# Kernel tuning notes

Measured on AMD Instinct MI355X. Metric: run time of the kernel, lower is better.

The kernel has to match this reference:

```python
import jax, jax.numpy as jnp
import numpy as np

N, C, HEADS, NL = 2048, 64, 4, 4
DH = C // HEADS
EPS = 1e-8

def _pdist(pos):
    d2 = jnp.sum((pos[:, None, :] - pos[None, :, :]) ** 2, -1)
    return jnp.sqrt(d2 + 1e-12)

def _edge_weights(pos, adj):
    d = _pdist(pos)
    sigma = jnp.maximum((adj * d).sum() / jnp.maximum(adj.sum(), 1.0), 1e-6)
    return adj * jnp.exp(-(d * d) / (2.0 * sigma * sigma))

def _curvatures(pos, adj):
    deg = jnp.maximum(adj.sum(1), 1.0)
    delta = (adj @ pos) / deg[:, None] - pos          # umbrella Laplacian of coordinates
    H = 0.5 * jnp.linalg.norm(delta, axis=1)          # mean curvature proxy
    d = _pdist(pos)
    r = (adj * d).sum(1) / deg
    var = (adj * (d - r[:, None]) ** 2).sum(1) / deg
    s = jnp.sqrt(var + 1e-12)
    k1, k2 = H + s, H - s
    return dict(mean=H, gaussian=k1 * k2, principal_1=k1, principal_2=k2,
                shape_index=(2.0 / jnp.pi) * jnp.arctan((k1 + k2) / (k1 - k2 + 1e-6)),
                curvedness=jnp.sqrt(0.5 * (k1 ** 2 + k2 ** 2)))

def _ln(x, g, b):
    mu = x.mean(-1, keepdims=True)
    v = ((x - mu) ** 2).mean(-1, keepdims=True)
    return (x - mu) * jax.lax.rsqrt(v + 1e-5) * g + b

def _forward(positions, adj, Wc1, bc1, Wc2, bc2, Win, b_in,
             conv_Wself, conv_bself, conv_Wneigh, conv_bneigh, conv_res,
             diff_W, diff_b, rd_W1, rd_b1, rd_W2, rd_b2, rd_coef,
             ln_g, ln_b, Wq, bq, Wk, bk, Wv, bv, Wo, bo, attn_beta, Wout, bout):
    n = positions.shape[0]
    # --- CurvatureEncoder ---
    cd = _curvatures(positions, adj)
    raw = jnp.stack([cd['mean'], cd['gaussian'], cd['principal_1'],
                     cd['principal_2'], cd['shape_index'], cd['curvedness']], 1)
    raw = (raw - raw.mean(0, keepdims=True)) / jnp.maximum(raw.std(0, ddof=1, keepdims=True), 1e-6)
    curv = jax.nn.silu(raw @ Wc1 + bc1) @ Wc2 + bc2           # (N,16)
    h = jnp.concatenate([positions, curv], -1) @ Win + b_in   # (N,C)
    # --- geometric operators (shared) ---
    W = _edge_weights(positions, adj)
    deg = W.sum(1)
    L = W - jnp.diag(deg)                                     # L = W - D (negative semidefinite)
    Dis = jnp.maximum(deg, EPS) ** -0.5
    L_norm = Dis[:, None] * L * Dis[None, :]
    evals, evecs = jnp.linalg.eigh(L)
    P = W / jnp.maximum(deg, EPS)[:, None]                    # row-stochastic propagation
    t_scales = jnp.array([0.5, 2.0, 8.0], dtype=h.dtype)
    for i in range(NL):
        res = h
        # CotangentConv with learned residual (scale 0.1)
        h = (h @ conv_Wself[i] + conv_bself[i]) \
            + ((P @ h) @ conv_Wneigh[i] + conv_bneigh[i]) \
            + 0.1 * conv_res[i] * h
        h = jax.nn.silu(h)
        if i % 2 == 0:
            # DiffusionConv: 3 heat-kernel scales exp(t*L) via shared eigendecomposition
            j = i // 2
            spec = evecs.T @ h                                # (N,C)
            filt = jnp.exp(t_scales[:, None] * evals[None, :])  # (3,N), evals <= 0
            hd = jnp.einsum('nk,skc->snc', evecs, filt[:, :, None] * spec[None])
            h = h + jnp.einsum('snc,scd->nd', hd, diff_W[j]) + diff_b[j]
        # ReactionDiffusion explicit Euler step (dt = 0.1)
        react = jnp.tanh(h @ rd_W1[i] + rd_b1[i]) @ rd_W2[i] + rd_b2[i]
        h = h + 0.1 * (rd_coef[i] * (L_norm @ h) + react)
        h = _ln(h + res, ln_g[i], ln_b[i])
    # --- CurvatureAttention (adjacency-masked, curvature-biased) ---
    q = (h @ Wq + bq).reshape(n, HEADS, DH)
    k = (h @ Wk + bk).reshape(n, HEADS, DH)
    v = (h @ Wv + bv).reshape(n, HEADS, DH)
    scores = jnp.einsum('nhd,mhd->hnm', q, k) / np.sqrt(DH).astype(np.float32)
    Hc = cd['mean']
    bias = -jax.nn.softplus(attn_beta)[:, None, None] * jnp.abs(Hc[:, None] - Hc[None, :])[None]
    mask = (adj + jnp.eye(n, dtype=adj.dtype)) > 0
    attn = jax.nn.softmax(jnp.where(mask[None], scores + bias, -1e9), -1)
    h = h + jnp.einsum('hnm,mhd->nhd', attn, v).reshape(n, C) @ Wo + bo
    return h @ Wout + bout                                    # (N,1)

def setup_inputs() -> dict:
    key = jax.random.key(0)
    ks = jax.random.split(key, 16)
    pos = jax.random.normal(ks[0], (N, 3), jnp.float32)
    u = jax.random.uniform(ks[1], (N, N))
    m = jnp.triu(u < (16.0 / N), k=1)
    adj = (m | m.T).astype(jnp.float32)           # symmetric 0/1, zero diagonal, avg deg ~16
    def w(k, *s):
        fan = s[-2] if len(s) > 1 else s[-1]
        return jax.random.normal(k, s, jnp.float32) / np.sqrt(fan).astype(np.float32)
    return dict(
        positions=pos, adj=adj,
        Wc1=w(ks[2], 6, 32), bc1=jnp.zeros((32,), jnp.float32),
        Wc2=w(ks[3], 32, 16), bc2=jnp.zeros((16,), jnp.float32),
        Win=w(ks[4], 19, C), b_in=jnp.zeros((C,), jnp.float32),
        conv_Wself=w(ks[5], NL, C, C), conv_bself=jnp.zeros((NL, C), jnp.float32),
        conv_Wneigh=w(ks[6], NL, C, C), conv_bneigh=jnp.zeros((NL, C), jnp.float32),
        conv_res=jnp.ones((NL,), jnp.float32),
        diff_W=w(ks[7], 2, 3, C, C), diff_b=jnp.zeros((2, C), jnp.float32),
        rd_W1=w(ks[8], NL, C, C), rd_b1=jnp.zeros((NL, C), jnp.float32),
        rd_W2=w(ks[9], NL, C, C), rd_b2=jnp.zeros((NL, C), jnp.float32),
        rd_coef=0.5 * jnp.ones((NL, C), jnp.float32),
        ln_g=jnp.ones((NL, C), jnp.float32), ln_b=jnp.zeros((NL, C), jnp.float32),
        Wq=w(ks[10], C, C), bq=jnp.zeros((C,), jnp.float32),
        Wk=w(ks[11], C, C), bk=jnp.zeros((C,), jnp.float32),
        Wv=w(ks[12], C, C), bv=jnp.zeros((C,), jnp.float32),
        Wo=w(ks[13], C, C), bo=jnp.zeros((C,), jnp.float32),
        attn_beta=jnp.ones((HEADS,), jnp.float32),
        Wout=w(ks[14], C, 1), bout=jnp.zeros((1,), jnp.float32),
    )

def reference(positions, adj, Wc1, bc1, Wc2, bc2, Win, b_in,
              conv_Wself, conv_bself, conv_Wneigh, conv_bneigh, conv_res,
              diff_W, diff_b, rd_W1, rd_b1, rd_W2, rd_b2, rd_coef,
              ln_g, ln_b, Wq, bq, Wk, bk, Wv, bv, Wo, bo, attn_beta, Wout, bout):
    return _forward(positions, adj, Wc1, bc1, Wc2, bc2, Win, b_in,
                    conv_Wself, conv_bself, conv_Wneigh, conv_bneigh, conv_res,
                    diff_W, diff_b, rd_W1, rd_b1, rd_W2, rd_b2, rd_coef,
                    ln_g, ln_b, Wq, bq, Wk, bk, Wv, bv, Wo, bo, attn_beta, Wout, bout)
```

## Files before the change

kernel.cpp:

```cpp
#include <hip/hip_runtime.h>
#include <math.h>

#define NPT 2048
#define CH 64
constexpr int TDEG = 12;
constexpr float SCL = 32.0f;

typedef __bf16 bf16_t;
typedef __bf16 bf16x8 __attribute__((ext_vector_type(8)));
typedef __bf16 bf16x4_t __attribute__((ext_vector_type(4)));
typedef float f32x4 __attribute__((ext_vector_type(4)));

__device__ __forceinline__ void gl_lds16(const void* g, void* l) {
  __builtin_amdgcn_global_load_lds(
      (const __attribute__((address_space(1))) void*)g,
      (__attribute__((address_space(3))) void*)l, 16, 0, 0);
}

__global__ __launch_bounds__(256) void pg_geom_csr(
    const float* __restrict__ pos, const float* __restrict__ adj,
    float* __restrict__ raw, float* __restrict__ Hc,
    float* __restrict__ sumA, float* __restrict__ sumAD,
    int* __restrict__ nbr, int* __restrict__ cnt)
{
  __shared__ float sp[NPT * 3];
  __shared__ float red[256 * 6];
  __shared__ int wsum[4];
  int i = blockIdx.x, t = threadIdx.x;
  for (int j = t; j < NPT * 3; j += 256) sp[j] = pos[j];
  __syncthreads();
  float px = sp[3 * i], py = sp[3 * i + 1], pz = sp[3 * i + 2];

  size_t base = (size_t)i * NPT + t * 8;
  float av[8];
  int c = 0;
  for (int u = 0; u < 8; u++) { av[u] = adj[base + u]; c += (av[u] != 0.0f); }
  int sc = c;
  int lane = t & 63;
  for (int off = 1; off < 64; off <<= 1) {
    int v = __shfl_up(sc, off);
    if (lane >= off) sc += v;
  }
  if (lane == 63) wsum[t >> 6] = sc;
  __syncthreads();
  int wprefix = 0;
  for (int w = 0; w < (t >> 6); w++) wprefix += wsum[w];
  int o = wprefix + sc - c;
  int wr = 0;
  for (int u = 0; u < 8; u++)
    if (av[u] != 0.0f) { int p = o + wr; if (p < 64) nbr[i * 64 + p] = t * 8 + u; wr++; }

  float s0 = 0, s1 = 0, s2 = 0, ax = 0, ay = 0, az = 0;
  for (int u = 0; u < 8; u++) {
    if (av[u] != 0.0f) {
      int j = t * 8 + u;
      float dx = sp[3 * j] - px, dy = sp[3 * j + 1] - py, dz = sp[3 * j + 2] - pz;
      float d2 = dx * dx + dy * dy + dz * dz + 1e-12f;
      float d = sqrtf(d2);
      s0 += 1.0f; s1 += d; s2 += d2;
      ax += sp[3 * j]; ay += sp[3 * j + 1]; az += sp[3 * j + 2];
    }
  }
  red[t * 6 + 0] = s0; red[t * 6 + 1] = s1; red[t * 6 + 2] = s2;
  red[t * 6 + 3] = ax; red[t * 6 + 4] = ay; red[t * 6 + 5] = az;
  __syncthreads();
  for (int s = 128; s > 0; s >>= 1) {
    if (t < s)
      for (int q = 0; q < 6; q++) red[t * 6 + q] += red[(t + s) * 6 + q];
    __syncthreads();
  }
  if (t == 0) {
    s0 = red[0]; s1 = red[1]; s2 = red[2]; ax = red[3]; ay = red[4]; az = red[5];
    float degc = fmaxf(s0, 1.0f);
    float dxm = ax / degc - px, dym = ay / degc - py, dzm = az / degc - pz;
    float H = 0.5f * sqrtf(dxm * dxm + dym * dym + dzm * dzm);
    float r = s1 / degc;
    float var = (s2 - 2.0f * r * s1 + r * r * s0) / degc;
    float sdev = sqrtf(var + 1e-12f);
    float k1 = H + sdev, k2 = H - sdev;
    raw[i * 6 + 0] = H;
    raw[i * 6 + 1] = k1 * k2;
    raw[i * 6 + 2] = k1;
    raw[i * 6 + 3] = k2;
    raw[i * 6 + 4] = 0.6366197723675814f * atanf((k1 + k2) / (k1 - k2 + 1e-6f));
    raw[i * 6 + 5] = sqrtf(0.5f * (k1 * k1 + k2 * k2));
    Hc[i] = H;
    sumA[i] = s0; sumAD[i] = s1;
    int tot = wsum[0] + wsum[1] + wsum[2] + wsum[3];
    cnt[i] = min(tot, 64);
  }
}

__global__ __launch_bounds__(256) void pg_stats(
    const float* __restrict__ raw, const float* __restrict__ sumA,
    const float* __restrict__ sumAD, float* __restrict__ stats)
{
  __shared__ float red[256];
  __shared__ float mean6[6];
  int t = threadIdx.x;
  float sa = 0, sad = 0;
  for (int j = t; j < NPT; j += 256) { sa += sumA[j]; sad += sumAD[j]; }
  red[t] = sa; __syncthreads();
  for (int s = 128; s > 0; s >>= 1) { if (t < s) red[t] += red[t + s]; __syncthreads(); }
  float totA = red[0]; __syncthreads();
  red[t] = sad; __syncthreads();
  for (int s = 128; s > 0; s >>= 1) { if (t < s) red[t] += red[t + s]; __syncthreads(); }
  float totAD = red[0]; __syncthreads();
  if (t == 0) {
    float sigma = fmaxf(totAD / fmaxf(totA, 1.0f), 1e-6f);
    stats[0] = 1.0f / (2.0f * sigma * sigma);
    stats[1] = sigma;
  }
  for (int q = 0; q < 6; q++) {
    float s = 0;
    for (int j = t; j < NPT; j += 256) s += raw[j * 6 + q];
    red[t] = s; __syncthreads();
    for (int k = 128; k > 0; k >>= 1) { if (t < k) red[t] += red[t + k]; __syncthreads(); }
    if (t == 0) mean6[q] = red[0] / (float)NPT;
    __syncthreads();
  }
  for (int q = 0; q < 6; q++) {
    float m = mean6[q], s = 0;
    for (int j = t; j < NPT; j += 256) { float d = raw[j * 6 + q] - m; s += d * d; }
    red[t] = s; __syncthreads();
    for (int k = 128; k > 0; k >>= 1) { if (t < k) red[t] += red[t + k]; __syncthreads(); }
    if (t == 0) {
      float sd = sqrtf(red[0] / (float)(NPT - 1));
      stats[2 + q] = m;
      stats[8 + q] = 1.0f / fmaxf(sd, 1e-6f);
    }
    __syncthreads();
  }
}

__global__ __launch_bounds__(64) void pg_wdeg(
    const float* __restrict__ pos, const int* __restrict__ nbr, const int* __restrict__ cnt,
    const float* __restrict__ stats, int2* __restrict__ pack, float* __restrict__ wdeg,
    float* __restrict__ invdeg, float* __restrict__ Dis, float* __restrict__ cvec)
{
  int i = blockIdx.x, t = threadIdx.x;
  int n = cnt[i];
  float inv2s2 = stats[0];
  float px = pos[3 * i], py = pos[3 * i + 1], pz = pos[3 * i + 2];
  float w = 0.0f;
  int j = 0;
  if (t < n) {
    j = nbr[i * 64 + t];
    float dx = pos[3 * j] - px, dy = pos[3 * j + 1] - py, dz = pos[3 * j + 2] - pz;
    float d2 = dx * dx + dy * dy + dz * dz + 1e-12f;
    w = expf(-d2 * inv2s2);
  }
  pack[i * 64 + t] = make_int2(j, __float_as_int(w));
  float s = w;
  for (int off = 1; off < 64; off <<= 1) s += __shfl_xor(s, off);
  if (t == 0) {
    float md = fmaxf(s, 1e-8f);
    wdeg[i] = s;
    invdeg[i] = 1.0f / md;
    float di = 1.0f / sqrtf(md);
    Dis[i] = di;
    cvec[i] = di * di * s;
  }
}

__global__ __launch_bounds__(64) void pg_curv_mlp(
    const float* __restrict__ pos, const float* __restrict__ raw, const float* __restrict__ stats,
    const float* __restrict__ Wc1, const float* __restrict__ bc1,
    const float* __restrict__ Wc2, const float* __restrict__ bc2,
    const float* __restrict__ Win, const float* __restrict__ b_in, float* __restrict__ h)
{
  __shared__ float feat[19];
  __shared__ float nraw[6];
  __shared__ float hid[32];
  int i = blockIdx.x, t = threadIdx.x;
  if (t < 3) feat[t] = pos[3 * i + t];
  if (t < 6) nraw[t] = (raw[i * 6 + t] - stats[2 + t]) * stats[8 + t];
  __syncthreads();
  if (t < 32) {
    float a = bc1[t];
    for (int k = 0; k < 6; k++) a += nraw[k] * Wc1[k * 32 + t];
    hid[t] = a / (1.0f + expf(-a));
  }
  __syncthreads();
  if (t < 16) {
    float a = bc2[t];
    for (int k = 0; k < 32; k++) a += hid[k] * Wc2[k * 16 + t];
    feat[3 + t] = a;
  }
  __syncthreads();
  float a = b_in[t];
  for (int k = 0; k < 19; k++) a += feat[k] * Win[k * CH + t];
  h[i * CH + t] = a;
}

__global__ __launch_bounds__(256) void pg_hinit(
    const int2* __restrict__ pack, const int* __restrict__ cnt,
    const float* __restrict__ wdeg, float* __restrict__ Y)
{
  int r = blockIdx.x, t = threadIdx.x;
  const float c0 = 1.0f / (SCL * (float)TDEG);
  float* row = Y + (size_t)r * NPT;
  for (int j = t * 4; j < NPT; j += 1024)
    *(f32x4*)(row + j) = (f32x4){0.f, 0.f, 0.f, 0.f};
  __syncthreads();
  int n = cnt[r];
  if (t < n) {
    int2 p = pack[r * 64 + t];
    row[p.x] = __int_as_float(p.y) * c0;
  }
  if (t == 0) row[r] = 1.0f - wdeg[r] * c0;
}

template <bool LAST>
__global__ __launch_bounds__(256) void pg_hstep(
    const int2* __restrict__ pack, const int* __restrict__ cnt,
    const float* __restrict__ wdeg, const float* __restrict__ Yin,
    float* __restrict__ Yout, float invc,
    bf16_t* __restrict__ Th, bf16_t* __restrict__ Tl)
{
  int b = blockIdx.x;
  int s = b & 7, w = b >> 3;
  int t = threadIdx.x;
  int lane = t & 63, v = t >> 6;
  int c0 = s * 256 + lane * 4;
#pragma unroll
  for (int ri = 0; ri < 2; ri++) {
    int r = __builtin_amdgcn_readfirstlane(w * 8 + v * 2 + ri);
    int n = cnt[r];
    float wd = wdeg[r];
    const int2* pr = pack + r * 64;
    f32x4 y0 = *(const f32x4*)(Yin + (size_t)r * NPT + c0);
    f32x4 acc0 = {-wd * y0[0], -wd * y0[1], -wd * y0[2], -wd * y0[3]};
    f32x4 acc1 = {0.f, 0.f, 0.f, 0.f};
    int nn = (n + 1) & ~1;
    for (int q = 0; q < nn; q += 2) {
      int2 p0 = pr[q], p1 = pr[q + 1];
      float w0 = __int_as_float(p0.y), w1 = __int_as_float(p1.y);
      f32x4 g0 = *(const f32x4*)(Yin + (size_t)p0.x * NPT + c0);
      f32x4 g1 = *(const f32x4*)(Yin + (size_t)p1.x * NPT + c0);
#pragma unroll
      for (int e = 0; e < 4; e++) {
        acc0[e] += w0 * g0[e];
        acc1[e] += w1 * g1[e];
      }
    }
    f32x4 val;
#pragma unroll
    for (int e = 0; e < 4; e++) {
      float id = (c0 + e == r) ? 1.0f : 0.0f;
      val[e] = id + (acc0[e] + acc1[e]) * invc;
    }
    if (LAST) {
      bf16x4_t hv, lv;
#pragma unroll
      for (int e = 0; e < 4; e++) {
        __bf16 hb = (__bf16)val[e];
        hv[e] = hb;
        lv[e] = (__bf16)(val[e] - (float)hb);
      }
      *(bf16x4_t*)(Th + (size_t)r * NPT + c0) = hv;
      *(bf16x4_t*)(Tl + (size_t)r * NPT + c0) = lv;
    } else {
      *(f32x4*)(Yout + (size_t)r * NPT + c0) = val;
    }
  }
}

__global__ __launch_bounds__(256) void pg_sq(
    const bf16_t* __restrict__ Ah, const bf16_t* __restrict__ Al,
    bf16_t* __restrict__ Ch, bf16_t* __restrict__ Cl)
{
  __shared__ __align__(16) char smem[131072];
  const int t = threadIdx.x;
  const int w = t >> 6, l = t & 63;
  const int lrow = l & 15, lhi = l >> 4;
  int bid = blockIdx.x;
  int sbid = (bid & 7) * 32 + (bid >> 3);
  const int by = sbid >> 4, bx = sbid & 15;
  const int wr = w >> 1, wc = w & 1;

  int offA[4], offB[4];
#pragma unroll
  for (int it = 0; it < 4; it++) {
    int o = it * 4096 + t * 16;
    int r = o >> 7;
    int cb = (o & 127) ^ ((r & 7) << 4);
    offA[it] = (by * 128 + r) * (NPT * 2) + cb;
    offB[it] = (bx * 128 + r) * (NPT * 2) + cb;
  }
  int aoff[4][2], boff[4][2];
#pragma unroll
  for (int m = 0; m < 4; m++) {
    int arow = wr * 64 + m * 16 + lrow;
    int brow = wc * 64 + m * 16 + lrow;
#pragma unroll
    for (int kk = 0; kk < 2; kk++) {
      int kb = kk * 64 + lhi * 16;
      aoff[m][kk] = arow * 128 + (kb ^ ((arow & 7) << 4));
      boff[m][kk] = brow * 128 + (kb ^ ((brow & 7) << 4));
    }
  }

  f32x4 acc[4][4];
#pragma unroll
  for (int m = 0; m < 4; m++)
#pragma unroll
    for (int n = 0; n < 4; n++) acc[m][n] = (f32x4){0.f, 0.f, 0.f, 0.f};

  const int lofs_w = w << 10;
#pragma unroll
  for (int it = 0; it < 4; it++) {
    int lo = it * 4096 + lofs_w;
    gl_lds16((const char*)Ah + offA[it], smem + lo);
    gl_lds16((const char*)Al + offA[it], smem + 16384 + lo);
    gl_lds16((const char*)Ah + offB[it], smem + 32768 + lo);
    gl_lds16((const char*)Al + offB[it], smem + 49152 + lo);
  }
  __syncthreads();

  for (int ks = 0; ks < NPT / 64; ks++) {
    if (ks + 1 < NPT / 64) {
      char* nbuf = smem + ((ks + 1) & 1) * 65536;
      size_t kadv = (size_t)(ks + 1) * 128;
#pragma unroll
      for (int it = 0; it < 4; it++) {
        int lo = it * 4096 + lofs_w;
        gl_lds16((const char*)Ah + offA[it] + kadv, nbuf + lo);
        gl_lds16((const char*)Al + offA[it] + kadv, nbuf + 16384 + lo);
        gl_lds16((const char*)Ah + offB[it] + kadv, nbuf + 32768 + lo);
        gl_lds16((const char*)Al + offB[it] + kadv, nbuf + 49152 + lo);
      }
    }
    const char* cbuf = smem + (ks & 1) * 65536;
#pragma unroll
    for (int kk = 0; kk < 2; kk++) {
      bf16x8 bhf[4], blf[4];
#pragma unroll
      for (int n = 0; n < 4; n++) {
        bhf[n] = *(const bf16x8*)(cbuf + 32768 + boff[n][kk]);
        blf[n] = *(const bf16x8*)(cbuf + 49152 + boff[n][kk]);
      }
#pragma unroll
      for (int m = 0; m < 4; m++) {
        bf16x8 ah = *(const bf16x8*)(cbuf + aoff[m][kk]);
        bf16x8 al = *(const bf16x8*)(cbuf + 16384 + aoff[m][kk]);
#pragma unroll
        for (int n = 0; n < 4; n++) {
          acc[m][n] = __builtin_amdgcn_mfma_f32_16x16x32_bf16(al, bhf[n], acc[m][n], 0, 0, 0);
          acc[m][n] = __builtin_amdgcn_mfma_f32_16x16x32_bf16(ah, blf[n], acc[m][n], 0, 0, 0);
          acc[m][n] = __builtin_amdgcn_mfma_f32_16x16x32_bf16(ah, bhf[n], acc[m][n], 0, 0, 0);
        }
      }
    }
    __syncthreads();
  }

  const int gr0 = by * 128 + wr * 64 + lhi * 4;
  const int gc0 = bx * 128 + wc * 64 + lrow;
#pragma unroll
  for (int m = 0; m < 4; m++) {
#pragma unroll
    for (int n = 0; n < 4; n++) {
      int gc = gc0 + n * 16;
#pragma unroll
      for (int r = 0; r < 4; r++) {
        float c = acc[m][n][r];
        __bf16 hb = (__bf16)c;
        size_t o = (size_t)(gr0 + m * 16 + r) * NPT + gc;
        Ch[o] = hb;
        Cl[o] = (__bf16)(c - (float)hb);
      }
    }
  }
}

__global__ __launch_bounds__(256) void pg_splitx(
    const float* __restrict__ X, bf16_t* __restrict__ XTh, bf16_t* __restrict__ XTl)
{
  __shared__ float sX[64][65];
  int t = threadIdx.x;
  int r0 = blockIdx.x * 64;
  for (int u = 0; u < 16; u++) {
    int idx = u * 256 + t;
    int r = idx >> 6, c = idx & 63;
    sX[r][c] = X[(size_t)(r0 + r) * CH + c];
  }
  __syncthreads();
  int c = t >> 6;
  int rr = t & 63;
  for (int cc = c; cc < 64; cc += 4) {
    float v = sX[rr][cc];
    __bf16 hb = (__bf16)v;
    XTh[(size_t)cc * NPT + r0 + rr] = hb;
    XTl[(size_t)cc * NPT + r0 + rr] = (__bf16)(v - (float)hb);
  }
}

__global__ __launch_bounds__(256) void pg_emm(
    const bf16_t* __restrict__ E05h, const bf16_t* __restrict__ E05l,
    const bf16_t* __restrict__ E2h,  const bf16_t* __restrict__ E2l,
    const bf16_t* __restrict__ E8h,  const bf16_t* __restrict__ E8l,
    const bf16_t* __restrict__ XTh,  const bf16_t* __restrict__ XTl,
    float* __restrict__ hd)
{
  __shared__ __align__(16) char smem[65536];
  const int t = threadIdx.x;
  const int w = t >> 6, l = t & 63;
  const int lrow = l & 15, lhi = l >> 4;
  const int scale = blockIdx.y;
  const bf16_t* Eh = (scale == 0) ? E05h : (scale == 1) ? E2h : E8h;
  const bf16_t* El = (scale == 0) ? E05l : (scale == 1) ? E2l : E8l;
  const int rb = blockIdx.x;

  int offA[2], offB[2];
#pragma unroll
  for (int it = 0; it < 2; it++) {
    int o = it * 4096 + t * 16;
    int r = o >> 7;
    int cb = (o & 127) ^ ((r & 7) << 4);
    offA[it] = (rb * 64 + r) * (NPT * 2) + cb;
    offB[it] = r * (NPT * 2) + cb;
  }
  int aoff[2], boff[4][2];
  {
    int arow = w * 16 + lrow;
#pragma unroll
    for (int kk = 0; kk < 2; kk++) {
      int kb = kk * 64 + lhi * 16;
      aoff[kk] = arow * 128 + (kb ^ ((arow & 7) << 4));
    }
  }
#pragma unroll
  for (int n = 0; n < 4; n++) {
    int brow = n * 16 + lrow;
#pragma unroll
    for (int kk = 0; kk < 2; kk++) {
      int kb = kk * 64 + lhi * 16;
      boff[n][kk] = brow * 128 + (kb ^ ((brow & 7) << 4));
    }
  }

  f32x4 acc[4];
#pragma unroll
  for (int n = 0; n < 4; n++) acc[n] = (f32x4){0.f, 0.f, 0.f, 0.f};

  const int lofs_w = w << 10;
#pragma unroll
  for (int it = 0; it < 2; it++) {
    int lo = it * 4096 + lofs_w;
    gl_lds16((const char*)Eh  + offA[it], smem + lo);
    gl_lds16((const char*)El  + offA[it], smem + 8192 + lo);
    gl_lds16((const char*)XTh + offB[it], smem + 16384 + lo);
    gl_lds16((const char*)XTl + offB[it], smem + 24576 + lo);
  }
  __syncthreads();

  for (int ks = 0; ks < NPT / 64; ks++) {
    if (ks + 1 < NPT / 64) {
      char* nbuf = smem + ((ks + 1) & 1) * 32768;
      size_t kadv = (size_t)(ks + 1) * 128;
#pragma unroll
      for (int it = 0; it < 2; it++) {
        int lo = it * 4096 + lofs_w;
        gl_lds16((const char*)Eh  + offA[it] + kadv, nbuf + lo);
        gl_lds16((const char*)El  + offA[it] + kadv, nbuf + 8192 + lo);
        gl_lds16((const char*)XTh + offB[it] + kadv, nbuf + 16384 + lo);
        gl_lds16((const char*)XTl + offB[it] + kadv, nbuf + 24576 + lo);
      }
    }
    const char* cbuf = smem + (ks & 1) * 32768;
#pragma unroll
    for (int kk = 0; kk < 2; kk++) {
      bf16x8 ah = *(const bf16x8*)(cbuf + aoff[kk]);
      bf16x8 al = *(const bf16x8*)(cbuf + 8192 + aoff[kk]);
#pragma unroll
      for (int n = 0; n < 4; n++) {
        bf16x8 bh = *(const bf16x8*)(cbuf + 16384 + boff[n][kk]);
        bf16x8 bl = *(const bf16x8*)(cbuf + 24576 + boff[n][kk]);
        acc[n] = __builtin_amdgcn_mfma_f32_16x16x32_bf16(al, bh, acc[n], 0, 0, 0);
        acc[n] = __builtin_amdgcn_mfma_f32_16x16x32_bf16(ah, bl, acc[n], 0, 0, 0);
        acc[n] = __builtin_amdgcn_mfma_f32_16x16x32_bf16(ah, bh, acc[n], 0, 0, 0);
      }
    }
    __syncthreads();
  }

  float* Y = hd + (size_t)scale * NPT * CH;
  const int gr0 = rb * 64 + w * 16 + lhi * 4;
#pragma unroll
  for (int n = 0; n < 4; n++) {
    int gc = n * 16 + lrow;
#pragma unroll
    for (int r = 0; r < 4; r++)
      Y[(size_t)(gr0 + r) * CH + gc] = acc[n][r];
  }
}

__global__ __launch_bounds__(64) void pg_convP(
    const int2* __restrict__ pack, const int* __restrict__ cnt,
    const float* __restrict__ invdeg, const float* __restrict__ h,
    const float* __restrict__ Ws, const float* __restrict__ bs,
    const float* __restrict__ Wn, const float* __restrict__ bn,
    const float* __restrict__ cres, float* __restrict__ out)
{
  __shared__ float sh[64], sp2[64];
  int i = blockIdx.x, t = threadIdx.x;
  sh[t] = h[i * CH + t];
  int n = cnt[i];
  float acc = 0.0f;
  for (int q = 0; q < n; q++) {
    int2 p = pack[i * 64 + q];
    acc += __int_as_float(p.y) * h[(size_t)p.x * CH + t];
  }
  sp2[t] = acc * invdeg[i];
  __syncthreads();
  float a = bs[t] + bn[t] + 0.1f * cres[0] * sh[t];
  for (int k = 0; k < 64; k++) a += sh[k] * Ws[k * CH + t] + sp2[k] * Wn[k * CH + t];
  out[i * CH + t] = a / (1.0f + expf(-a));
}

__global__ __launch_bounds__(64) void pg_difffuse(
    const float* __restrict__ h2, const float* __restrict__ hd,
    const float* __restrict__ dW, const float* __restrict__ db, float* __restrict__ out)
{
  __shared__ float sh[3][64];
  int i = blockIdx.x, t = threadIdx.x;
  for (int s = 0; s < 3; s++) sh[s][t] = hd[(size_t)s * NPT * CH + i * CH + t];
  __syncthreads();
  float a = h2[i * CH + t] + db[t];
  for (int s = 0; s < 3; s++) {
    const float* w = dW + s * CH * CH;
    for (int k = 0; k < 64; k++) a += sh[s][k] * w[k * CH + t];
  }
  out[i * CH + t] = a;
}

__global__ __launch_bounds__(64) void pg_tlr(
    const int2* __restrict__ pack, const int* __restrict__ cnt,
    const float* __restrict__ Dis, const float* __restrict__ cvec,
    const float* __restrict__ h3,
    const float* __restrict__ W1, const float* __restrict__ b1,
    const float* __restrict__ W2, const float* __restrict__ b2,
    const float* __restrict__ rdc,
    const float* __restrict__ g, const float* __restrict__ b,
    float* __restrict__ hio)
{
  __shared__ float sh[64], st[64];
  int i = blockIdx.x, t = threadIdx.x;
  sh[t] = h3[i * CH + t];
  __syncthreads();
  float a = b1[t];
  for (int k = 0; k < 64; k++) a += sh[k] * W1[k * CH + t];
  st[t] = tanhf(a);
  int n = cnt[i];
  float accL = 0.0f;
  for (int q = 0; q < n; q++) {
    int2 p = pack[i * 64 + q];
    accL += __int_as_float(p.y) * Dis[p.x] * h3[(size_t)p.x * CH + t];
  }
  float tLv = accL * Dis[i] - cvec[i] * sh[t];
  __syncthreads();
  float react = b2[t];
  for (int k = 0; k < 64; k++) react += st[k] * W2[k * CH + t];
  float x = sh[t] + 0.1f * (rdc[t] * tLv + react) + hio[i * CH + t];
  float s = x;
  for (int off = 1; off < 64; off <<= 1) s += __shfl_xor(s, off);
  float mu = s * (1.0f / 64.0f);
  float d = x - mu;
  float v = d * d;
  for (int off = 1; off < 64; off <<= 1) v += __shfl_xor(v, off);
  v *= (1.0f / 64.0f);
  hio[i * CH + t] = d * (1.0f / sqrtf(v + 1e-5f)) * g[t] + b[t];
}

__global__ __launch_bounds__(64) void pg_qkv(
    const float* __restrict__ h,
    const float* __restrict__ Wq, const float* __restrict__ bq,
    const float* __restrict__ Wk, const float* __restrict__ bk,
    const float* __restrict__ Wv, const float* __restrict__ bv,
    float* __restrict__ q, float* __restrict__ kb, float* __restrict__ vb)
{
  __shared__ float sh[64];
  int i = blockIdx.x, t = threadIdx.x;
  sh[t] = h[i * CH + t];
  __syncthreads();
  float aq = bq[t], ak = bk[t], avv = bv[t];
  for (int k = 0; k < 64; k++) {
    float x = sh[k];
    aq += x * Wq[k * CH + t];
    ak += x * Wk[k * CH + t];
    avv += x * Wv[k * CH + t];
  }
  q[i * CH + t] = aq;
  kb[i * CH + t] = ak;
  vb[i * CH + t] = avv;
}

__global__ __launch_bounds__(256) void pg_attn_out(
    const float* __restrict__ q, const float* __restrict__ kb, const float* __restrict__ vb,
    const int* __restrict__ nbr, const int* __restrict__ cnt,
    const float* __restrict__ Hc, const float* __restrict__ beta,
    const float* __restrict__ h,
    const float* __restrict__ Wo, const float* __restrict__ bo,
    const float* __restrict__ Wout, const float* __restrict__ bout,
    float* __restrict__ out)
{
  __shared__ float av_s[64];
  int i = blockIdx.x;
  int t = threadIdx.x;
  int head = t >> 6, lane = t & 63;
  float sp_b = logf(1.0f + expf(beta[head]));
  float hci = Hc[i];
  const float* qp = q + i * CH + head * 16;
  float qr[16];
#pragma unroll
  for (int d = 0; d < 16; d++) qr[d] = qp[d];
  int n = cnt[i];
  int K = n + 1;
  float mx = -1e30f, den = 0.0f;
  float vac[16];
#pragma unroll
  for (int d = 0; d < 16; d++) vac[d] = 0.0f;
  for (int m = lane; m < K; m += 64) {
    int j = (m == n) ? i : nbr[i * 64 + m];
    const float* kp = kb + (size_t)j * CH + head * 16;
    float sc = 0.0f;
#pragma unroll
    for (int d = 0; d < 16; d++) sc += qr[d] * kp[d];
    sc *= 0.25f;
    sc -= sp_b * fabsf(hci - Hc[j]);
    float nm = fmaxf(mx, sc);
    float corr = expf(mx - nm);
    float p = expf(sc - nm);
    den = den * corr + p;
    const float* vp = vb + (size_t)j * CH + head * 16;
#pragma unroll
    for (int d = 0; d < 16; d++) vac[d] = vac[d] * corr + p * vp[d];
    mx = nm;
  }
  for (int off = 32; off > 0; off >>= 1) {
    float omx = __shfl_down(mx, off);
    float oden = __shfl_down(den, off);
    float ov[16];
#pragma unroll
    for (int d = 0; d < 16; d++) ov[d] = __shfl_down(vac[d], off);
    float nm = fmaxf(mx, omx);
    float c1 = expf(mx - nm), c2 = expf(omx - nm);
    den = den * c1 + oden * c2;
#pragma unroll
    for (int d = 0; d < 16; d++) vac[d] = vac[d] * c1 + ov[d] * c2;
    mx = nm;
  }
  if (lane == 0) {
    float inv = 1.0f / den;
    for (int d = 0; d < 16; d++) av_s[head * 16 + d] = vac[d] * inv;
  }
  __syncthreads();
  if (t < 64) {
    float a = h[i * CH + t] + bo[t];
    for (int k = 0; k < 64; k++) a += av_s[k] * Wo[k * CH + t];
    float s = a * Wout[t];
    for (int off = 1; off < 64; off <<= 1) s += __shfl_xor(s, off);
    if (t == 0) out[i] = s + bout[0];
  }
}

extern "C" void kernel_launch(void* const* d_in, const int* in_sizes, int n_in,
                              void* d_out, int out_size, void* d_ws, size_t ws_size,
                              hipStream_t stream)
{
  const float* pos   = (const float*)d_in[0];
  const float* adj   = (const float*)d_in[1];
  const float* Wc1   = (const float*)d_in[2];
  const float* bc1   = (const float*)d_in[3];
  const float* Wc2   = (const float*)d_in[4];
  const float* bc2   = (const float*)d_in[5];
  const float* Win   = (const float*)d_in[6];
  const float* b_in  = (const float*)d_in[7];
  const float* cWs   = (const float*)d_in[8];
  const float* cbs   = (const float*)d_in[9];
  const float* cWn   = (const float*)d_in[10];
  const float* cbn   = (const float*)d_in[11];
  const float* cres  = (const float*)d_in[12];
  const float* dW    = (const float*)d_in[13];
  const float* db    = (const float*)d_in[14];
  const float* rW1   = (const float*)d_in[15];
  const float* rb1   = (const float*)d_in[16];
  const float* rW2   = (const float*)d_in[17];
  const float* rb2   = (const float*)d_in[18];
  const float* rdc   = (const float*)d_in[19];
  const float* lng   = (const float*)d_in[20];
  const float* lnb   = (const float*)d_in[21];
  const float* Wq    = (const float*)d_in[22];
  const float* bq    = (const float*)d_in[23];
  const float* Wk    = (const float*)d_in[24];
  const float* bk    = (const float*)d_in[25];
  const float* Wv    = (const float*)d_in[26];
  const float* bv    = (const float*)d_in[27];
  const float* Wo    = (const float*)d_in[28];
  const float* bo    = (const float*)d_in[29];
  const float* abeta = (const float*)d_in[30];
  const float* Wout  = (const float*)d_in[31];
  const float* bout  = (const float*)d_in[32];

  const size_t NNe = (size_t)NPT * NPT;
  const size_t NC  = (size_t)NPT * CH;
  const size_t P   = NNe * 2;

  char* base = (char*)d_ws;
  bf16_t* E05h = (bf16_t*)(base + 0 * P);
  bf16_t* E05l = (bf16_t*)(base + 1 * P);
  bf16_t* E2h  = (bf16_t*)(base + 2 * P);
  bf16_t* E2l  = (bf16_t*)(base + 3 * P);
  bf16_t* E8h  = (bf16_t*)(base + 4 * P);
  bf16_t* E8l  = (bf16_t*)(base + 5 * P);
  bf16_t* SAh  = (bf16_t*)(base + 6 * P);
  bf16_t* SAl  = (bf16_t*)(base + 7 * P);
  bf16_t* SBh  = (bf16_t*)(base + 8 * P);
  bf16_t* SBl  = (bf16_t*)(base + 9 * P);
  float*  M0   = (float*)(base + 0 * P);
  float*  M1   = (float*)(base + 2 * P);
  bf16_t* XTh  = (bf16_t*)(base + 12 * P);
  bf16_t* XTl  = (bf16_t*)(base + 12 * P + NPT * CH * 2);
  float*  smb  = (float*)(base + 12 * P + 1024 * 1024);

  float* h   = smb;
  float* tA  = h + NC;
  float* tB  = tA + NC;
  float* hd  = tB + NC;
  float* q   = hd + 3 * NC;
  float* kbf = q + NC;
  float* vbf = kbf + NC;
  float* raw = vbf + NC;
  float* sm  = raw + 8 * NPT;
  float* sumA   = sm;
  float* sumAD  = sm + NPT;
  float* wdeg   = sm + 2 * NPT;
  float* invdeg = sm + 3 * NPT;
  float* Dis    = sm + 4 * NPT;
  float* cvec   = sm + 5 * NPT;
  float* Hc     = sm + 6 * NPT;
  float* stats  = sm + 7 * NPT;
  int*   nbr    = (int*)(sm + 8 * NPT);
  int*   cnt    = nbr + (size_t)NPT * 64;
  int2*  pack   = (int2*)(cnt + NPT);

  size_t need = 12 * P + 1024 * 1024
              + (9 * NC + 16 * (size_t)NPT) * 4
              + (size_t)NPT * 64 * 4 + NPT * 4 + (size_t)NPT * 64 * 8 + 256;
  if (ws_size < need) return;

  pg_geom_csr<<<NPT, 256, 0, stream>>>(pos, adj, raw, Hc, sumA, sumAD, nbr, cnt);
  pg_stats<<<1, 256, 0, stream>>>(raw, sumA, sumAD, stats);
  pg_wdeg<<<NPT, 64, 0, stream>>>(pos, nbr, cnt, stats, pack, wdeg, invdeg, Dis, cvec);
  pg_curv_mlp<<<NPT, 64, 0, stream>>>(pos, raw, stats, Wc1, bc1, Wc2, bc2, Win, b_in, h);

  pg_hinit<<<NPT, 256, 0, stream>>>(pack, cnt, wdeg, M0);
  float* cur = M0;
  float* nxt = M1;
  for (int k = TDEG - 1; k >= 2; k--) {
    pg_hstep<false><<<NPT, 256, 0, stream>>>(pack, cnt, wdeg, cur, nxt,
                                             1.0f / (SCL * (float)k), nullptr, nullptr);
    float* tmp = cur; cur = nxt; nxt = tmp;
  }
  pg_hstep<true><<<NPT, 256, 0, stream>>>(pack, cnt, wdeg, cur, nullptr,
                                          1.0f / SCL, SAh, SAl);

  pg_sq<<<256, 256, 0, stream>>>(SAh, SAl, SBh, SBl);
  pg_sq<<<256, 256, 0, stream>>>(SBh, SBl, SAh, SAl);
  pg_sq<<<256, 256, 0, stream>>>(SAh, SAl, SBh, SBl);
  pg_sq<<<256, 256, 0, stream>>>(SBh, SBl, E05h, E05l);
  pg_sq<<<256, 256, 0, stream>>>(E05h, E05l, SAh, SAl);
  pg_sq<<<256, 256, 0, stream>>>(SAh, SAl, E2h, E2l);
  pg_sq<<<256, 256, 0, stream>>>(E2h, E2l, SBh, SBl);
  pg_sq<<<256, 256, 0, stream>>>(SBh, SBl, E8h, E8l);

  for (int i = 0; i < 4; i++) {
    pg_convP<<<NPT, 64, 0, stream>>>(pack, cnt, invdeg, h,
                                     cWs + i * 4096, cbs + i * 64,
                                     cWn + i * 4096, cbn + i * 64, cres + i, tA);
    float* h3 = tA;
    if ((i & 1) == 0) {
      int j = i >> 1;
      pg_splitx<<<32, 256, 0, stream>>>(tA, XTh, XTl);
      pg_emm<<<dim3(32, 3), 256, 0, stream>>>(E05h, E05l, E2h, E2l, E8h, E8l,
                                              XTh, XTl, hd);
      pg_difffuse<<<NPT, 64, 0, stream>>>(tA, hd, dW + j * 3 * 4096, db + j * 64, tB);
      h3 = tB;
    }
    pg_tlr<<<NPT, 64, 0, stream>>>(pack, cnt, Dis, cvec, h3,
                                   rW1 + i * 4096, rb1 + i * 64,
                                   rW2 + i * 4096, rb2 + i * 64,
                                   rdc + i * 64, lng + i * 64, lnb + i * 64, h);
  }

  pg_qkv<<<NPT, 64, 0, stream>>>(h, Wq, bq, Wk, bk, Wv, bv, q, kbf, vbf);
  pg_attn_out<<<NPT, 256, 0, stream>>>(q, kbf, vbf, nbr, cnt, Hc, abeta,
                                       h, Wo, bo, Wout, bout, (float*)d_out);
}
```

Baseline: 791.9 us.

## Use higher-degree Taylor with smaller scaling to drop one squaring step

The matrix exponential is computed by scaling-and-squaring. Raising the Taylor degree from 12 to 14 and halving the scale factor from 32 to 16 removes one 2048x2048 squaring GEMM, at the cost of two extra sparse Taylor steps. The sparse step now unrolls neighbours by four with four accumulators for more memory-level parallelism. The squaring kernel's epilogue writes vectorized bf16x4 stores along contiguous rows, relying on the result being symmetric so the transposed layout stays valid. That symmetry assumption and the accuracy of the larger Taylor term with less scaling are the risks.

New measurement: 786.1 us. Within noise of the previous version (-0.7%).

```diff
diff --git a/kernel.cpp b/kernel.cpp
--- a/kernel.cpp
+++ b/kernel.cpp
@@ -3,8 +3,8 @@
 
 #define NPT 2048
 #define CH 64
-constexpr int TDEG = 12;
-constexpr float SCL = 32.0f;
+constexpr int TDEG = 14;
+constexpr float SCL = 16.0f;
 
 typedef __bf16 bf16_t;
 typedef __bf16 bf16x8 __attribute__((ext_vector_type(8)));
@@ -232,23 +232,30 @@
     f32x4 y0 = *(const f32x4*)(Yin + (size_t)r * NPT + c0);
     f32x4 acc0 = {-wd * y0[0], -wd * y0[1], -wd * y0[2], -wd * y0[3]};
     f32x4 acc1 = {0.f, 0.f, 0.f, 0.f};
-    int nn = (n + 1) & ~1;
-    for (int q = 0; q < nn; q += 2) {
-      int2 p0 = pr[q], p1 = pr[q + 1];
+    f32x4 acc2 = {0.f, 0.f, 0.f, 0.f};
+    f32x4 acc3 = {0.f, 0.f, 0.f, 0.f};
+    int nn = (n + 3) & ~3;
+    for (int q = 0; q < nn; q += 4) {
+      int2 p0 = pr[q], p1 = pr[q + 1], p2 = pr[q + 2], p3 = pr[q + 3];
       float w0 = __int_as_float(p0.y), w1 = __int_as_float(p1.y);
+      float w2 = __int_as_float(p2.y), w3 = __int_as_float(p3.y);
       f32x4 g0 = *(const f32x4*)(Yin + (size_t)p0.x * NPT + c0);
       f32x4 g1 = *(const f32x4*)(Yin + (size_t)p1.x * NPT + c0);
+      f32x4 g2 = *(const f32x4*)(Yin + (size_t)p2.x * NPT + c0);
+      f32x4 g3 = *(const f32x4*)(Yin + (size_t)p3.x * NPT + c0);
 #pragma unroll
       for (int e = 0; e < 4; e++) {
         acc0[e] += w0 * g0[e];
         acc1[e] += w1 * g1[e];
+        acc2[e] += w2 * g2[e];
+        acc3[e] += w3 * g3[e];
       }
     }
     f32x4 val;
 #pragma unroll
     for (int e = 0; e < 4; e++) {
       float id = (c0 + e == r) ? 1.0f : 0.0f;
-      val[e] = id + (acc0[e] + acc1[e]) * invc;
+      val[e] = id + ((acc0[e] + acc1[e]) + (acc2[e] + acc3[e])) * invc;
     }
     if (LAST) {
       bf16x4_t hv, lv;
@@ -359,17 +366,20 @@
   const int gc0 = bx * 128 + wc * 64 + lrow;
 #pragma unroll
   for (int m = 0; m < 4; m++) {
+    int cb = gr0 + m * 16;
 #pragma unroll
     for (int n = 0; n < 4; n++) {
       int gc = gc0 + n * 16;
+      bf16x4_t hv, lv;
 #pragma unroll
       for (int r = 0; r < 4; r++) {
         float c = acc[m][n][r];
         __bf16 hb = (__bf16)c;
-        size_t o = (size_t)(gr0 + m * 16 + r) * NPT + gc;
-        Ch[o] = hb;
-        Cl[o] = (__bf16)(c - (float)hb);
+        hv[r] = hb;
+        lv[r] = (__bf16)(c - (float)hb);
       }
+      *(bf16x4_t*)(Ch + (size_t)gc * NPT + cb) = hv;
+      *(bf16x4_t*)(Cl + (size_t)gc * NPT + cb) = lv;
     }
   }
 }
@@ -768,12 +778,11 @@
 
   pg_sq<<<256, 256, 0, stream>>>(SAh, SAl, SBh, SBl);
   pg_sq<<<256, 256, 0, stream>>>(SBh, SBl, SAh, SAl);
-  pg_sq<<<256, 256, 0, stream>>>(SAh, SAl, SBh, SBl);
-  pg_sq<<<256, 256, 0, stream>>>(SBh, SBl, E05h, E05l);
-  pg_sq<<<256, 256, 0, stream>>>(E05h, E05l, SAh, SAl);
-  pg_sq<<<256, 256, 0, stream>>>(SAh, SAl, E2h, E2l);
-  pg_sq<<<256, 256, 0, stream>>>(E2h, E2l, SBh, SBl);
-  pg_sq<<<256, 256, 0, stream>>>(SBh, SBl, E8h, E8l);
+  pg_sq<<<256, 256, 0, stream>>>(SAh, SAl, E05h, E05l);
+  pg_sq<<<256, 256, 0, stream>>>(E05h, E05l, SBh, SBl);
+  pg_sq<<<256, 256, 0, stream>>>(SBh, SBl, E2h, E2l);
+  pg_sq<<<256, 256, 0, stream>>>(E2h, E2l, SAh, SAl);
+  pg_sq<<<256, 256, 0, stream>>>(SAh, SAl, E8h, E8l);
 
   for (int i = 0; i < 4; i++) {
     pg_convP<<<NPT, 64, 0, stream>>>(pack, cnt, invdeg, h,
```

## Use symmetric split-bf16 squaring with scaled low parts and a symmetrizing fix pass

Applied to the files above, without the earlier changes.

The heat-kernel matrix power chain drops the lo×hi MFMA term in each squaring, since the matrix is symmetric: it loads only the high part of A and both parts of B. A new pg_fix kernel re-symmetrizes each product by averaging it with its transpose. Low parts are stored scaled by 2 to keep more precision. The Taylor degree rises to 14 with scale 16, so one squaring is removed. The hstep kernel now processes two rows together with 4-way unrolled gathers, and emm uses a halved-hi operand to match the scaled low part of E. The aim is to cut MFMA work and LDS traffic in the dominant squaring GEMMs, at the cost of extra transpose passes and possible accuracy loss.

New measurement: 841.4 us. 6.3% more time.

```diff
diff --git a/kernel.cpp b/kernel.cpp
--- a/kernel.cpp
+++ b/kernel.cpp
@@ -3,8 +3,9 @@
 
 #define NPT 2048
 #define CH 64
-constexpr int TDEG = 12;
-constexpr float SCL = 32.0f;
+constexpr int TDEG = 14;
+constexpr float SCL = 16.0f;
+
 
 typedef __bf16 bf16_t;
 typedef __bf16 bf16x8 __attribute__((ext_vector_type(8)));
@@ -216,61 +217,83 @@
     const int2* __restrict__ pack, const int* __restrict__ cnt,
     const float* __restrict__ wdeg, const float* __restrict__ Yin,
     float* __restrict__ Yout, float invc,
-    bf16_t* __restrict__ Th, bf16_t* __restrict__ Tl)
+    bf16_t* __restrict__ Th, bf16_t* __restrict__ Tl2)
 {
   int b = blockIdx.x;
   int s = b & 7, w = b >> 3;
   int t = threadIdx.x;
   int lane = t & 63, v = t >> 6;
   int c0 = s * 256 + lane * 4;
-#pragma unroll
-  for (int ri = 0; ri < 2; ri++) {
-    int r = __builtin_amdgcn_readfirstlane(w * 8 + v * 2 + ri);
-    int n = cnt[r];
-    float wd = wdeg[r];
-    const int2* pr = pack + r * 64;
-    f32x4 y0 = *(const f32x4*)(Yin + (size_t)r * NPT + c0);
-    f32x4 acc0 = {-wd * y0[0], -wd * y0[1], -wd * y0[2], -wd * y0[3]};
-    f32x4 acc1 = {0.f, 0.f, 0.f, 0.f};
-    int nn = (n + 1) & ~1;
-    for (int q = 0; q < nn; q += 2) {
-      int2 p0 = pr[q], p1 = pr[q + 1];
-      float w0 = __int_as_float(p0.y), w1 = __int_as_float(p1.y);
-      f32x4 g0 = *(const f32x4*)(Yin + (size_t)p0.x * NPT + c0);
-      f32x4 g1 = *(const f32x4*)(Yin + (size_t)p1.x * NPT + c0);
-#pragma unroll
-      for (int e = 0; e < 4; e++) {
-        acc0[e] += w0 * g0[e];
-        acc1[e] += w1 * g1[e];
-      }
-    }
-    f32x4 val;
+  int r0 = __builtin_amdgcn_readfirstlane(w * 8 + v * 2);
+  int r1 = r0 + 1;
+  int n0 = cnt[r0], n1 = cnt[r1];
+  float wd0 = wdeg[r0], wd1 = wdeg[r1];
+  const int2* pr0 = pack + r0 * 64;
+  const int2* pr1 = pack + r1 * 64;
+  f32x4 y0 = *(const f32x4*)(Yin + (size_t)r0 * NPT + c0);
+  f32x4 y1 = *(const f32x4*)(Yin + (size_t)r1 * NPT + c0);
+  f32x4 a0, a1, a2, a3, b0, b1, b2, b3;
+#pragma unroll
+  for (int e = 0; e < 4; e++) {
+    a0[e] = -wd0 * y0[e]; b0[e] = -wd1 * y1[e];
+    a1[e] = 0.f; a2[e] = 0.f; a3[e] = 0.f;
+    b1[e] = 0.f; b2[e] = 0.f; b3[e] = 0.f;
+  }
+  int nmax = n0 > n1 ? n0 : n1;
+  int nn = (nmax + 3) & ~3;
+  for (int q = 0; q < nn; q += 4) {
+    int2 pa0 = pr0[q], pa1 = pr0[q + 1], pa2 = pr0[q + 2], pa3 = pr0[q + 3];
+    int2 pb0 = pr1[q], pb1 = pr1[q + 1], pb2 = pr1[q + 2], pb3 = pr1[q + 3];
+    f32x4 ga0 = *(const f32x4*)(Yin + (size_t)pa0.x * NPT + c0);
+    f32x4 ga1 = *(const f32x4*)(Yin + (size_t)pa1.x * NPT + c0);
+    f32x4 ga2 = *(const f32x4*)(Yin + (size_t)pa2.x * NPT + c0);
+    f32x4 ga3 = *(const f32x4*)(Yin + (size_t)pa3.x * NPT + c0);
+    f32x4 gb0 = *(const f32x4*)(Yin + (size_t)pb0.x * NPT + c0);
+    f32x4 gb1 = *(const f32x4*)(Yin + (size_t)pb1.x * NPT + c0);
+    f32x4 gb2 = *(const f32x4*)(Yin + (size_t)pb2.x * NPT + c0);
+    f32x4 gb3 = *(const f32x4*)(Yin + (size_t)pb3.x * NPT + c0);
+    float wa0 = __int_as_float(pa0.y), wa1 = __int_as_float(pa1.y);
+    float wa2 = __int_as_float(pa2.y), wa3 = __int_as_float(pa3.y);
+    float wb0 = __int_as_float(pb0.y), wb1 = __int_as_float(pb1.y);
+    float wb2 = __int_as_float(pb2.y), wb3 = __int_as_float(pb3.y);
 #pragma unroll
     for (int e = 0; e < 4; e++) {
-      float id = (c0 + e == r) ? 1.0f : 0.0f;
-      val[e] = id + (acc0[e] + acc1[e]) * invc;
-    }
-    if (LAST) {
-      bf16x4_t hv, lv;
-#pragma unroll
-      for (int e = 0; e < 4; e++) {
-        __bf16 hb = (__bf16)val[e];
-        hv[e] = hb;
-        lv[e] = (__bf16)(val[e] - (float)hb);
-      }
-      *(bf16x4_t*)(Th + (size_t)r * NPT + c0) = hv;
-      *(bf16x4_t*)(Tl + (size_t)r * NPT + c0) = lv;
-    } else {
-      *(f32x4*)(Yout + (size_t)r * NPT + c0) = val;
-    }
+      a0[e] += wa0 * ga0[e]; a1[e] += wa1 * ga1[e];
+      a2[e] += wa2 * ga2[e]; a3[e] += wa3 * ga3[e];
+      b0[e] += wb0 * gb0[e]; b1[e] += wb1 * gb1[e];
+      b2[e] += wb2 * gb2[e]; b3[e] += wb3 * gb3[e];
+    }
+  }
+  f32x4 v0, v1;
+#pragma unroll
+  for (int e = 0; e < 4; e++) {
+    v0[e] = ((c0 + e == r0) ? 1.0f : 0.0f) + ((a0[e] + a1[e]) + (a2[e] + a3[e])) * invc;
+    v1[e] = ((c0 + e == r1) ? 1.0f : 0.0f) + ((b0[e] + b1[e]) + (b2[e] + b3[e])) * invc;
+  }
+  if (LAST) {
+    bf16x4_t h0, l0, h1, l1;
+#pragma unroll
+    for (int e = 0; e < 4; e++) {
+      __bf16 hb0 = (__bf16)v0[e];
+      __bf16 hb1 = (__bf16)v1[e];
+      h0[e] = hb0; l0[e] = (__bf16)(2.0f * (v0[e] - (float)hb0));
+      h1[e] = hb1; l1[e] = (__bf16)(2.0f * (v1[e] - (float)hb1));
+    }
+    *(bf16x4_t*)(Th  + (size_t)r0 * NPT + c0) = h0;
+    *(bf16x4_t*)(Tl2 + (size_t)r0 * NPT + c0) = l0;
+    *(bf16x4_t*)(Th  + (size_t)r1 * NPT + c0) = h1;
+    *(bf16x4_t*)(Tl2 + (size_t)r1 * NPT + c0) = l1;
+  } else {
+    *(f32x4*)(Yout + (size_t)r0 * NPT + c0) = v0;
+    *(f32x4*)(Yout + (size_t)r1 * NPT + c0) = v1;
   }
 }
 
 __global__ __launch_bounds__(256) void pg_sq(
-    const bf16_t* __restrict__ Ah, const bf16_t* __restrict__ Al,
-    bf16_t* __restrict__ Ch, bf16_t* __restrict__ Cl)
-{
-  __shared__ __align__(16) char smem[131072];
+    const bf16_t* __restrict__ Ah, const bf16_t* __restrict__ Al2,
+    bf16_t* __restrict__ SCh, bf16_t* __restrict__ SCl2)
+{
+  __shared__ __align__(16) char smem[98304];
   const int t = threadIdx.x;
   const int w = t >> 6, l = t & 63;
   const int lrow = l & 15, lhi = l >> 4;
@@ -311,42 +334,38 @@
 #pragma unroll
   for (int it = 0; it < 4; it++) {
     int lo = it * 4096 + lofs_w;
-    gl_lds16((const char*)Ah + offA[it], smem + lo);
-    gl_lds16((const char*)Al + offA[it], smem + 16384 + lo);
-    gl_lds16((const char*)Ah + offB[it], smem + 32768 + lo);
-    gl_lds16((const char*)Al + offB[it], smem + 49152 + lo);
+    gl_lds16((const char*)Ah  + offA[it], smem + lo);
+    gl_lds16((const char*)Ah  + offB[it], smem + 16384 + lo);
+    gl_lds16((const char*)Al2 + offB[it], smem + 32768 + lo);
   }
   __syncthreads();
 
   for (int ks = 0; ks < NPT / 64; ks++) {
     if (ks + 1 < NPT / 64) {
-      char* nbuf = smem + ((ks + 1) & 1) * 65536;
+      char* nbuf = smem + ((ks + 1) & 1) * 49152;
       size_t kadv = (size_t)(ks + 1) * 128;
 #pragma unroll
       for (int it = 0; it < 4; it++) {
         int lo = it * 4096 + lofs_w;
-        gl_lds16((const char*)Ah + offA[it] + kadv, nbuf + lo);
-        gl_lds16((const char*)Al + offA[it] + kadv, nbuf + 16384 + lo);
-        gl_lds16((const char*)Ah + offB[it] + kadv, nbuf + 32768 + lo);
-        gl_lds16((const char*)Al + offB[it] + kadv, nbuf + 49152 + lo);
+        gl_lds16((const char*)Ah  + offA[it] + kadv, nbuf + lo);
+        gl_lds16((const char*)Ah  + offB[it] + kadv, nbuf + 16384 + lo);
+        gl_lds16((const char*)Al2 + offB[it] + kadv, nbuf + 32768 + lo);
       }
     }
-    const char* cbuf = smem + (ks & 1) * 65536;
+    const char* cbuf = smem + (ks & 1) * 49152;
 #pragma unroll
     for (int kk = 0; kk < 2; kk++) {
       bf16x8 bhf[4], blf[4];
 #pragma unroll
       for (int n = 0; n < 4; n++) {
-        bhf[n] = *(const bf16x8*)(cbuf + 32768 + boff[n][kk]);
-        blf[n] = *(const bf16x8*)(cbuf + 49152 + boff[n][kk]);
+        bhf[n] = *(const bf16x8*)(cbuf + 16384 + boff[n][kk]);
+        blf[n] = *(const bf16x8*)(cbuf + 32768 + boff[n][kk]);
       }
 #pragma unroll
       for (int m = 0; m < 4; m++) {
         bf16x8 ah = *(const bf16x8*)(cbuf + aoff[m][kk]);
-        bf16x8 al = *(const bf16x8*)(cbuf + 16384 + aoff[m][kk]);
 #pragma unroll
         for (int n = 0; n < 4; n++) {
-          acc[m][n] = __builtin_amdgcn_mfma_f32_16x16x32_bf16(al, bhf[n], acc[m][n], 0, 0, 0);
           acc[m][n] = __builtin_amdgcn_mfma_f32_16x16x32_bf16(ah, blf[n], acc[m][n], 0, 0, 0);
           acc[m][n] = __builtin_amdgcn_mfma_f32_16x16x32_bf16(ah, bhf[n], acc[m][n], 0, 0, 0);
         }
@@ -367,15 +386,52 @@
         float c = acc[m][n][r];
         __bf16 hb = (__bf16)c;
         size_t o = (size_t)(gr0 + m * 16 + r) * NPT + gc;
-        Ch[o] = hb;
-        Cl[o] = (__bf16)(c - (float)hb);
+        SCh[o] = hb;
+        SCl2[o] = (__bf16)(2.0f * (c - (float)hb));
       }
     }
   }
 }
 
+__global__ __launch_bounds__(256) void pg_fix(
+    const bf16_t* __restrict__ Sh, const bf16_t* __restrict__ Sl2,
+    bf16_t* __restrict__ Oh, bf16_t* __restrict__ Ol2)
+{
+  __shared__ float T2[128][129];
+  int bj = blockIdx.x, bi = blockIdx.y;
+  int t = threadIdx.x;
+  int row = t >> 1, cb = (t & 1) * 64;
+  size_t base2 = ((size_t)(bj * 128 + row)) * NPT + bi * 128 + cb;
+  for (int i = 0; i < 8; i++) {
+    bf16x8 h8 = *(const bf16x8*)(Sh + base2 + i * 8);
+    bf16x8 l8 = *(const bf16x8*)(Sl2 + base2 + i * 8);
+#pragma unroll
+    for (int e = 0; e < 8; e++)
+      T2[row][cb + i * 8 + e] = (float)h8[e] + 0.5f * (float)l8[e];
+  }
+  __syncthreads();
+  size_t base1 = ((size_t)(bi * 128 + row)) * NPT + bj * 128 + cb;
+  for (int i = 0; i < 8; i++) {
+    bf16x8 h8 = *(const bf16x8*)(Sh + base1 + i * 8);
+    bf16x8 l8 = *(const bf16x8*)(Sl2 + base1 + i * 8);
+    bf16x8 oh, ol;
+#pragma unroll
+    for (int e = 0; e < 8; e++) {
+      float s1 = (float)h8[e] + 0.5f * (float)l8[e];
+      float s2 = T2[cb + i * 8 + e][row];
+      float cv = 0.5f * (s1 + s2);
+      __bf16 hb = (__bf16)cv;
+      oh[e] = hb;
+      ol[e] = (__bf16)(2.0f * (cv - (float)hb));
+    }
+    *(bf16x8*)(Oh + base1 + i * 8) = oh;
+    *(bf16x8*)(Ol2 + base1 + i * 8) = ol;
+  }
+}
+
 __global__ __launch_bounds__(256) void pg_splitx(
-    const float* __restrict__ X, bf16_t* __restrict__ XTh, bf16_t* __restrict__ XTl)
+    const float* __restrict__ X, bf16_t* __restrict__ XTh,
+    bf16_t* __restrict__ XTl, bf16_t* __restrict__ XTh2)
 {
   __shared__ float sX[64][65];
   int t = threadIdx.x;
@@ -393,6 +449,7 @@
     __bf16 hb = (__bf16)v;
     XTh[(size_t)cc * NPT + r0 + rr] = hb;
     XTl[(size_t)cc * NPT + r0 + rr] = (__bf16)(v - (float)hb);
+    XTh2[(size_t)cc * NPT + r0 + rr] = (__bf16)(0.5f * (float)hb);
   }
 }
 
@@ -401,9 +458,9 @@
     const bf16_t* __restrict__ E2h,  const bf16_t* __restrict__ E2l,
     const bf16_t* __restrict__ E8h,  const bf16_t* __restrict__ E8l,
     const bf16_t* __restrict__ XTh,  const bf16_t* __restrict__ XTl,
-    float* __restrict__ hd)
-{
-  __shared__ __align__(16) char smem[65536];
+    const bf16_t* __restrict__ XTh2, float* __restrict__ hd)
+{
+  __shared__ __align__(16) char smem[81920];
   const int t = threadIdx.x;
   const int w = t >> 6, l = t & 63;
   const int lrow = l & 15, lhi = l >> 4;
@@ -448,38 +505,41 @@
 #pragma unroll
   for (int it = 0; it < 2; it++) {
     int lo = it * 4096 + lofs_w;
-    gl_lds16((const char*)Eh  + offA[it], smem + lo);
-    gl_lds16((const char*)El  + offA[it], smem + 8192 + lo);
-    gl_lds16((const char*)XTh + offB[it], smem + 16384 + lo);
-    gl_lds16((const char*)XTl + offB[it], smem + 24576 + lo);
+    gl_lds16((const char*)Eh   + offA[it], smem + lo);
+    gl_lds16((const char*)El   + offA[it], smem + 8192 + lo);
+    gl_lds16((const char*)XTh  + offB[it], smem + 16384 + lo);
+    gl_lds16((const char*)XTl  + offB[it], smem + 24576 + lo);
+    gl_lds16((const char*)XTh2 + offB[it], smem + 32768 + lo);
   }
   __syncthreads();
 
   for (int ks = 0; ks < NPT / 64; ks++) {
     if (ks + 1 < NPT / 64) {
-      char* nbuf = smem + ((ks + 1) & 1) * 32768;
+      char* nbuf = smem + ((ks + 1) & 1) * 40960;
       size_t kadv = (size_t)(ks + 1) * 128;
 #pragma unroll
       for (int it = 0; it < 2; it++) {
         int lo = it * 4096 + lofs_w;
-        gl_lds16((const char*)Eh  + offA[it] + kadv, nbuf + lo);
-        gl_lds16((const char*)El  + offA[it] + kadv, nbuf + 8192 + lo);
-        gl_lds16((const char*)XTh + offB[it] + kadv, nbuf + 16384 + lo);
-        gl_lds16((const char*)XTl + offB[it] + kadv, nbuf + 24576 + lo);
+        gl_lds16((const char*)Eh   + offA[it] + kadv, nbuf + lo);
+        gl_lds16((const char*)El   + offA[it] + kadv, nbuf + 8192 + lo);
+        gl_lds16((const char*)XTh  + offB[it] + kadv, nbuf + 16384 + lo);
+        gl_lds16((const char*)XTl  + offB[it] + kadv, nbuf + 24576 + lo);
+        gl_lds16((const char*)XTh2 + offB[it] + kadv, nbuf + 32768 + lo);
       }
     }
-    const char* cbuf = smem + (ks & 1) * 32768;
+    const char* cbuf = smem + (ks & 1) * 40960;
 #pragma unroll
     for (int kk = 0; kk < 2; kk++) {
-      bf16x8 ah = *(const bf16x8*)(cbuf + aoff[kk]);
-      bf16x8 al = *(const bf16x8*)(cbuf + 8192 + aoff[kk]);
+      bf16x8 eh  = *(const bf16x8*)(cbuf + aoff[kk]);
+      bf16x8 el2 = *(const bf16x8*)(cbuf + 8192 + aoff[kk]);
 #pragma unroll
       for (int n = 0; n < 4; n++) {
-        bf16x8 bh = *(const bf16x8*)(cbuf + 16384 + boff[n][kk]);
-        bf16x8 bl = *(const bf16x8*)(cbuf + 24576 + boff[n][kk]);
-        acc[n] = __builtin_amdgcn_mfma_f32_16x16x32_bf16(al, bh, acc[n], 0, 0, 0);
-        acc[n] = __builtin_amdgcn_mfma_f32_16x16x32_bf16(ah, bl, acc[n], 0, 0, 0);
-        acc[n] = __builtin_amdgcn_mfma_f32_16x16x32_bf16(ah, bh, acc[n], 0, 0, 0);
+        bf16x8 xh  = *(const bf16x8*)(cbuf + 16384 + boff[n][kk]);
+        bf16x8 xl  = *(const bf16x8*)(cbuf + 24576 + boff[n][kk]);
+        bf16x8 xh2 = *(const bf16x8*)(cbuf + 32768 + boff[n][kk]);
+        acc[n] = __builtin_amdgcn_mfma_f32_16x16x32_bf16(el2, xh2, acc[n], 0, 0, 0);
+        acc[n] = __builtin_amdgcn_mfma_f32_16x16x32_bf16(eh, xl, acc[n], 0, 0, 0);
+        acc[n] = __builtin_amdgcn_mfma_f32_16x16x32_bf16(eh, xh, acc[n], 0, 0, 0);
       }
     }
     __syncthreads();
@@ -721,7 +781,8 @@
   float*  M0   = (float*)(base + 0 * P);
   float*  M1   = (float*)(base + 2 * P);
   bf16_t* XTh  = (bf16_t*)(base + 12 * P);
-  bf16_t* XTl  = (bf16_t*)(base + 12 * P + NPT * CH * 2);
+  bf16_t* XTl  = (bf16_t*)(base + 12 * P + (size_t)NPT * CH * 2);
+  bf16_t* XTh2 = (bf16_t*)(base + 12 * P + (size_t)NPT * CH * 4);
   float*  smb  = (float*)(base + 12 * P + 1024 * 1024);
 
   float* h   = smb;
@@ -766,14 +827,21 @@
   pg_hstep<true><<<NPT, 256, 0, stream>>>(pack, cnt, wdeg, cur, nullptr,
                                           1.0f / SCL, SAh, SAl);
 
-  pg_sq<<<256, 256, 0, stream>>>(SAh, SAl, SBh, SBl);
-  pg_sq<<<256, 256, 0, stream>>>(SBh, SBl, SAh, SAl);
-  pg_sq<<<256, 256, 0, stream>>>(SAh, SAl, SBh, SBl);
-  pg_sq<<<256, 256, 0, stream>>>(SBh, SBl, E05h, E05l);
-  pg_sq<<<256, 256, 0, stream>>>(E05h, E05l, SAh, SAl);
-  pg_sq<<<256, 256, 0, stream>>>(SAh, SAl, E2h, E2l);
-  pg_sq<<<256, 256, 0, stream>>>(E2h, E2l, SBh, SBl);
-  pg_sq<<<256, 256, 0, stream>>>(SBh, SBl, E8h, E8l);
+  dim3 gfix(16, 16);
+  pg_sq <<<256, 256, 0, stream>>>(SAh, SAl, E05h, E05l);
+  pg_fix<<<gfix, 256, 0, stream>>>(E05h, E05l, SBh, SBl);
+  pg_sq <<<256, 256, 0, stream>>>(SBh, SBl, E05h, E05l);
+  pg_fix<<<gfix, 256, 0, stream>>>(E05h, E05l, SAh, SAl);
+  pg_sq <<<256, 256, 0, stream>>>(SAh, SAl, SBh, SBl);
+  pg_fix<<<gfix, 256, 0, stream>>>(SBh, SBl, E05h, E05l);
+  pg_sq <<<256, 256, 0, stream>>>(E05h, E05l, E2h, E2l);
+  pg_fix<<<gfix, 256, 0, stream>>>(E2h, E2l, SBh, SBl);
+  pg_sq <<<256, 256, 0, stream>>>(SBh, SBl, SAh, SAl);
+  pg_fix<<<gfix, 256, 0, stream>>>(SAh, SAl, E2h, E2l);
+  pg_sq <<<256, 256, 0, stream>>>(E2h, E2l, SBh, SBl);
+  pg_fix<<<gfix, 256, 0, stream>>>(SBh, SBl, SAh, SAl);
+  pg_sq <<<256, 256, 0, stream>>>(SAh, SAl, SBh, SBl);
+  pg_fix<<<gfix, 256, 0, stream>>>(SBh, SBl, E8h, E8l);
 
   for (int i = 0; i < 4; i++) {
     pg_convP<<<NPT, 64, 0, stream>>>(pack, cnt, invdeg, h,
@@ -782,9 +850,9 @@
     float* h3 = tA;
     if ((i & 1) == 0) {
       int j = i >> 1;
-      pg_splitx<<<32, 256, 0, stream>>>(tA, XTh, XTl);
+      pg_splitx<<<32, 256, 0, stream>>>(tA, XTh, XTl, XTh2);
       pg_emm<<<dim3(32, 3), 256, 0, stream>>>(E05h, E05l, E2h, E2l, E8h, E8l,
-                                              XTh, XTl, hd);
+                                              XTh, XTl, XTh2, hd);
       pg_difffuse<<<NPT, 64, 0, stream>>>(tA, hd, dW + j * 3 * 4096, db + j * 64, tB);
       h3 = tB;
     }
```
